# Optimization experiments

Hardware: AMD Instinct MI355X
Metric: run time of the kernel (lower is better)

Reference implementation:

```python
import jax, jax.numpy as jnp
import numpy as np

N_NODES = 50000
N_EDGES = 800000
DIMS = [128, 128, 128, 64]  # in, hid1, hid2, out
EPS = 1e-12


def setup_inputs() -> dict:
    key = jax.random.key(0)
    ks = jax.random.split(key, 32)
    inp = {
        "x": jax.random.normal(ks[0], (N_NODES, DIMS[0]), dtype=jnp.float32),
        "edge_src": jax.random.randint(ks[1], (N_EDGES,), 0, N_NODES),
        "edge_dst": jax.random.randint(ks[2], (N_EDGES,), 0, N_NODES),
    }
    k = 3
    for l in range(3):
        din, dout = DIMS[l], DIMS[l + 1]
        s_in = 1.0 / np.sqrt(din)
        inp[f"Wp{l+1}"] = jax.random.uniform(ks[k], (din, din), jnp.float32, -s_in, s_in); k += 1
        inp[f"bp{l+1}"] = jax.random.uniform(ks[k], (din,), jnp.float32, -s_in, s_in); k += 1
        inp[f"Ws{l+1}"] = jax.random.uniform(ks[k], (din, dout), jnp.float32, -s_in, s_in); k += 1
        inp[f"Wn{l+1}"] = jax.random.uniform(ks[k], (din, dout), jnp.float32, -s_in, s_in); k += 1
        inp[f"b{l+1}"] = jnp.zeros((dout,), jnp.float32); k += 1
    return inp


def _sage_pool_layer(x, src, dst, Wp, bp, Ws, Wn, b):
    # per-edge: relu(fc_pool(x_src)); [E, din]
    m = jax.nn.relu(x[src] @ Wp + bp)
    # max-pool over in-neighbors of each dst node; [N, din]
    pooled = jax.ops.segment_max(m, dst, num_segments=x.shape[0])
    deg = jax.ops.segment_sum(jnp.ones((dst.shape[0],), x.dtype), dst,
                              num_segments=x.shape[0])
    pooled = jnp.where(deg[:, None] > 0, pooled, 0.0)  # zero-degree -> 0 (DGL)
    return x @ Ws + pooled @ Wn + b


def _l2norm_relu(h):
    n = jnp.sqrt(jnp.sum(h * h, axis=1, keepdims=True))
    return jax.nn.relu(h / jnp.maximum(n, EPS))


def reference(x, edge_src, edge_dst,
              Wp1, bp1, Ws1, Wn1, b1,
              Wp2, bp2, Ws2, Wn2, b2,
              Wp3, bp3, Ws3, Wn3, b3):
    h = _l2norm_relu(_sage_pool_layer(x, edge_src, edge_dst, Wp1, bp1, Ws1, Wn1, b1))
    h = _l2norm_relu(_sage_pool_layer(h, edge_src, edge_dst, Wp2, bp2, Ws2, Wn2, b2))
    h = _l2norm_relu(_sage_pool_layer(h, edge_src, edge_dst, Wp3, bp3, Ws3, Wn3, b3))
    return h
```

## Files before the change

### kernel.cpp

```cpp
#include <hip/hip_runtime.h>
#include <math.h>

#define N_NODES 50000
#define N_EDGES 800000
#define CAP 64
#define RANGES 8
#define NODES_PER_RANGE 6250
#define CSRB 1024
#define GEMMB 782
#define LROW 136

typedef __attribute__((ext_vector_type(8))) short short8;
typedef __attribute__((ext_vector_type(2))) short short2v;
typedef __attribute__((ext_vector_type(4))) float f32x4;

__device__ __forceinline__ unsigned short f2bf(float f) {
    unsigned int u = __float_as_uint(f);
    return (unsigned short)((u + 0x7FFFu + ((u >> 16) & 1u)) >> 16);
}

template <bool F32>
__device__ __forceinline__ short8 loadA(const void* A, int off) {
    short8 r;
    if (F32) {
        const float* p = (const float*)A + off;
        float4 f0 = *(const float4*)p;
        float4 f1 = *(const float4*)(p + 4);
        r[0] = (short)f2bf(f0.x); r[1] = (short)f2bf(f0.y);
        r[2] = (short)f2bf(f0.z); r[3] = (short)f2bf(f0.w);
        r[4] = (short)f2bf(f1.x); r[5] = (short)f2bf(f1.y);
        r[6] = (short)f2bf(f1.z); r[7] = (short)f2bf(f1.w);
    } else {
        r = *(const short8*)((const unsigned short*)A + off);
    }
    return r;
}

struct WDescs { const float* W[9]; int N[9]; };

__global__ __launch_bounds__(256) void prep_kernel(
    WDescs wd, unsigned short* __restrict__ Wpk, int* __restrict__ deg)
{
    const int nthr = gridDim.x * 256;
    const int tid = blockIdx.x * 256 + threadIdx.x;
    for (int id = tid; id < 9 * 16384; id += nthr) {
        int mi = id >> 14;
        int loc = id & 16383;
        int N = wd.N[mi];
        if (loc < 128 * N) {
            int c = loc / (N * 32);
            int n = (loc - c * N * 32) >> 5;
            int k = c * 32 + (loc & 31);
            Wpk[mi * 16384 + loc] = f2bf(wd.W[mi][k * N + n]);
        }
    }
    for (int i = tid; i < N_NODES; i += nthr) deg[i] = 0;
}

__global__ __launch_bounds__(256) void mix_kernel(
    const int* __restrict__ esrc, const int* __restrict__ edst,
    int* __restrict__ deg, unsigned short* __restrict__ csr16,
    const float* __restrict__ x, const unsigned short* __restrict__ Wp1,
    const float* __restrict__ bp1, unsigned short* __restrict__ Y)
{
    if (blockIdx.x < CSRB) {
        int range = blockIdx.x & (RANGES - 1);
        for (int cb = blockIdx.x >> 3; cb < N_EDGES / 256; cb += CSRB / 8) {
            int e = cb * 256 + threadIdx.x;
            int d = edst[e];
            if ((unsigned)(d - range * NODES_PER_RANGE) < (unsigned)NODES_PER_RANGE) {
                int r = atomicAdd(&deg[d], 1);
                if (r < CAP) csr16[(d << 6) + r] = (unsigned short)esrc[e];
            }
        }
        return;
    }
    const int tile = blockIdx.x - CSRB;
    const int lane = threadIdx.x & 63;
    const int wv = threadIdx.x >> 6;
    const int cl = lane & 15;
    const int quad = lane >> 4;
    const int rowBase = tile * 64 + wv * 16;
    const int ar = min(rowBase + cl, N_NODES - 1);
    const int bLane = cl * 32 + quad * 8;

    f32x4 acc[8];
    #pragma unroll
    for (int t = 0; t < 8; ++t) acc[t] = (f32x4){0.f, 0.f, 0.f, 0.f};

    #pragma unroll
    for (int c = 0; c < 4; ++c) {
        short8 af = loadA<true>(x, ar * 128 + c * 32 + quad * 8);
        const unsigned short* Bc = Wp1 + c * 4096 + bLane;
        #pragma unroll
        for (int t = 0; t < 8; ++t) {
            short8 bf = *(const short8*)(Bc + t * 512);
            acc[t] = __builtin_amdgcn_mfma_f32_16x16x32_bf16(af, bf, acc[t], 0, 0, 0);
        }
    }
    const int row0 = rowBase + quad * 4;
    #pragma unroll
    for (int t = 0; t < 8; ++t) {
        float bc = bp1[t * 16 + cl];
        #pragma unroll
        for (int g = 0; g < 4; ++g) {
            int r = row0 + g;
            if (r < N_NODES)
                Y[r * 128 + t * 16 + cl] = f2bf(fmaxf(acc[t][g] + bc, 0.0f));
        }
    }
}

template <bool A0F32, bool LAST>
__global__ __launch_bounds__(256) void pd_kernel(
    const void* __restrict__ A0,
    const unsigned short* __restrict__ B0, const unsigned short* __restrict__ B1,
    const float* __restrict__ bias,
    const unsigned short* __restrict__ Yin, const int* __restrict__ deg,
    const unsigned short* __restrict__ csr16,
    unsigned short* __restrict__ outH, float* __restrict__ outF,
    const unsigned short* __restrict__ Bnext, const float* __restrict__ bnext,
    unsigned short* __restrict__ Yout)
{
    constexpr int NT = LAST ? 4 : 8;
    constexpr int N = NT * 16;
    __shared__ unsigned short lds[4][16 * LROW];

    const int lane = threadIdx.x & 63;
    const int wv = threadIdx.x >> 6;
    const int cl = lane & 15;
    const int quad = lane >> 4;
    const int tile = blockIdx.x;
    const int nodeBase = tile * 64 + wv * 16;
    unsigned short* plw = &lds[wv][0];

    {
        const unsigned short* yb = Yin + 2 * lane;
        for (int j = 0; j < 16; ++j) {
            int n = min(nodeBase + j, N_NODES - 1);
            int e0 = n << 6;
            int e1 = e0 + min(deg[n], CAP);
            short2v acc = (short2v){0, 0};
            int e = e0;
            for (; e + 8 <= e1; e += 8) {
                int s0 = csr16[e + 0], s1 = csr16[e + 1];
                int s2 = csr16[e + 2], s3 = csr16[e + 3];
                int s4 = csr16[e + 4], s5 = csr16[e + 5];
                int s6 = csr16[e + 6], s7 = csr16[e + 7];
                short2v v0 = *(const short2v*)(yb + (s0 << 7));
                short2v v1 = *(const short2v*)(yb + (s1 << 7));
                short2v v2 = *(const short2v*)(yb + (s2 << 7));
                short2v v3 = *(const short2v*)(yb + (s3 << 7));
                short2v v4 = *(const short2v*)(yb + (s4 << 7));
                short2v v5 = *(const short2v*)(yb + (s5 << 7));
                short2v v6 = *(const short2v*)(yb + (s6 << 7));
                short2v v7 = *(const short2v*)(yb + (s7 << 7));
                acc = __builtin_elementwise_max(acc, v0);
                acc = __builtin_elementwise_max(acc, v1);
                acc = __builtin_elementwise_max(acc, v2);
                acc = __builtin_elementwise_max(acc, v3);
                acc = __builtin_elementwise_max(acc, v4);
                acc = __builtin_elementwise_max(acc, v5);
                acc = __builtin_elementwise_max(acc, v6);
                acc = __builtin_elementwise_max(acc, v7);
            }
            for (; e < e1; ++e) {
                int s = csr16[e];
                short2v v = *(const short2v*)(yb + (s << 7));
                acc = __builtin_elementwise_max(acc, v);
            }
            *(short2v*)(plw + j * LROW + 2 * lane) = acc;
        }
    }

    const int ar = min(nodeBase + cl, N_NODES - 1);
    const int bLane = cl * 32 + quad * 8;
    f32x4 acc[NT];
    #pragma unroll
    for (int t = 0; t < NT; ++t) acc[t] = (f32x4){0.f, 0.f, 0.f, 0.f};

    #pragma unroll
    for (int c = 0; c < 4; ++c) {
        short8 a0 = loadA<A0F32>(A0, ar * 128 + c * 32 + quad * 8);
        short8 a1 = *(const short8*)(plw + cl * LROW + c * 32 + quad * 8);
        const unsigned short* B0c = B0 + c * (N * 32) + bLane;
        const unsigned short* B1c = B1 + c * (N * 32) + bLane;
        #pragma unroll
        for (int t = 0; t < NT; ++t) {
            short8 bf = *(const short8*)(B0c + t * 512);
            acc[t] = __builtin_amdgcn_mfma_f32_16x16x32_bf16(a0, bf, acc[t], 0, 0, 0);
        }
        #pragma unroll
        for (int t = 0; t < NT; ++t) {
            short8 bf = *(const short8*)(B1c + t * 512);
            acc[t] = __builtin_amdgcn_mfma_f32_16x16x32_bf16(a1, bf, acc[t], 0, 0, 0);
        }
    }

    #pragma unroll
    for (int t = 0; t < NT; ++t) {
        float bc = bias[t * 16 + cl];
        #pragma unroll
        for (int g = 0; g < 4; ++g) acc[t][g] += bc;
    }

    float inv[4];
    #pragma unroll
    for (int g = 0; g < 4; ++g) {
        float s = 0.f;
        #pragma unroll
        for (int t = 0; t < NT; ++t) s += acc[t][g] * acc[t][g];
        s += __shfl_xor(s, 1, 64);
        s += __shfl_xor(s, 2, 64);
        s += __shfl_xor(s, 4, 64);
        s += __shfl_xor(s, 8, 64);
        inv[g] = 1.0f / fmaxf(sqrtf(s), 1e-12f);
    }

    const int row0 = nodeBase + quad * 4;

    if (LAST) {
        #pragma unroll
        for (int t = 0; t < NT; ++t)
            #pragma unroll
            for (int g = 0; g < 4; ++g) {
                int r = row0 + g;
                if (r < N_NODES)
                    outF[r * N + t * 16 + cl] = fmaxf(acc[t][g] * inv[g], 0.0f);
            }
        return;
    }

    #pragma unroll
    for (int t = 0; t < NT; ++t)
        #pragma unroll
        for (int g = 0; g < 4; ++g) {
            int r = row0 + g;
            unsigned short h = f2bf(fmaxf(acc[t][g] * inv[g], 0.0f));
            if (r < N_NODES) outH[r * 128 + t * 16 + cl] = h;
            plw[(quad * 4 + g) * LROW + t * 16 + cl] = h;
        }

    f32x4 ya[8];
    #pragma unroll
    for (int t = 0; t < 8; ++t) ya[t] = (f32x4){0.f, 0.f, 0.f, 0.f};
    #pragma unroll
    for (int c = 0; c < 4; ++c) {
        short8 af = *(const short8*)(plw + cl * LROW + c * 32 + quad * 8);
        const unsigned short* Bc = Bnext + c * 4096 + bLane;
        #pragma unroll
        for (int t = 0; t < 8; ++t) {
            short8 bf = *(const short8*)(Bc + t * 512);
            ya[t] = __builtin_amdgcn_mfma_f32_16x16x32_bf16(af, bf, ya[t], 0, 0, 0);
        }
    }
    #pragma unroll
    for (int t = 0; t < 8; ++t) {
        float bc = bnext[t * 16 + cl];
        #pragma unroll
        for (int g = 0; g < 4; ++g) {
            int r = row0 + g;
            if (r < N_NODES)
                Yout[r * 128 + t * 16 + cl] = f2bf(fmaxf(ya[t][g] + bc, 0.0f));
        }
    }
}

extern "C" void kernel_launch(void* const* d_in, const int* in_sizes, int n_in,
                              void* d_out, int out_size, void* d_ws, size_t ws_size,
                              hipStream_t stream) {
    const float* x    = (const float*)d_in[0];
    const int*   esrc = (const int*)d_in[1];
    const int*   edst = (const int*)d_in[2];
    const float* Wp[3], *bp[3], *Ws[3], *Wn[3], *bb[3];
    for (int l = 0; l < 3; ++l) {
        Wp[l] = (const float*)d_in[3 + 5 * l];
        bp[l] = (const float*)d_in[4 + 5 * l];
        Ws[l] = (const float*)d_in[5 + 5 * l];
        Wn[l] = (const float*)d_in[6 + 5 * l];
        bb[l] = (const float*)d_in[7 + 5 * l];
    }

    const int NF = N_NODES * 128;
    unsigned short* YA  = (unsigned short*)d_ws;
    unsigned short* YB  = YA + NF;
    unsigned short* H1  = YB + NF;
    unsigned short* H2  = H1 + NF;
    unsigned short* Wpk = H2 + NF;
    int* deg = (int*)(Wpk + 9 * 16384);
    unsigned short* csr16 = (unsigned short*)(deg + N_NODES);

    auto WH = [&](int i) { return Wpk + i * 16384; };

    WDescs wd;
    wd.W[0] = Wp[0]; wd.N[0] = 128;
    wd.W[1] = Ws[0]; wd.N[1] = 128;
    wd.W[2] = Wn[0]; wd.N[2] = 128;
    wd.W[3] = Wp[1]; wd.N[3] = 128;
    wd.W[4] = Ws[1]; wd.N[4] = 128;
    wd.W[5] = Wn[1]; wd.N[5] = 128;
    wd.W[6] = Wp[2]; wd.N[6] = 128;
    wd.W[7] = Ws[2]; wd.N[7] = 64;
    wd.W[8] = Wn[2]; wd.N[8] = 64;

    prep_kernel<<<576, 256, 0, stream>>>(wd, Wpk, deg);
    mix_kernel<<<CSRB + GEMMB, 256, 0, stream>>>(esrc, edst, deg, csr16,
                                                 x, WH(0), bp[0], YA);
    pd_kernel<true, false><<<GEMMB, 256, 0, stream>>>(
        x, WH(1), WH(2), bb[0], YA, deg, csr16, H1, nullptr, WH(3), bp[1], YB);
    pd_kernel<false, false><<<GEMMB, 256, 0, stream>>>(
        H1, WH(4), WH(5), bb[1], YB, deg, csr16, H2, nullptr, WH(6), bp[2], YA);
    pd_kernel<false, true><<<GEMMB, 256, 0, stream>>>(
        H2, WH(7), WH(8), bb[2], YA, deg, csr16, nullptr, (float*)d_out,
        nullptr, nullptr, nullptr);
}
```

Measured before the change: 390.8 us.

## Split neighbor max-pool into separate per-node kernel before dual GEMM

The neighbor max-pooling gather is pulled out of the fused pool+GEMM kernel into its own kernel. That kernel gives each node a wavefront and launches 12500 blocks, so many more gathers are in flight than in the 782-block fused kernel, where each wave walked 16 nodes one after another. The GEMM kernel then reads the pooled rows from a global buffer instead of LDS. The cost is an extra global write and read of the pooled tensor per layer, plus three more kernel launches.

```diff
diff --git a/kernel.cpp b/kernel.cpp
--- a/kernel.cpp
+++ b/kernel.cpp
@@ -111,13 +111,55 @@
     }
 }
 
+__global__ __launch_bounds__(256) void pool_max8(
+    const unsigned short* __restrict__ y, const int* __restrict__ deg,
+    const unsigned short* __restrict__ csr16, unsigned short* __restrict__ pool)
+{
+    const int wv = threadIdx.x >> 6;
+    const int d = threadIdx.x & 63;
+    const int n = blockIdx.x * 4 + wv;
+    const int e0 = n << 6;
+    const int e1 = e0 + min(deg[n], CAP);
+    const unsigned short* yb = y + 2 * d;
+
+    short2v acc = (short2v){0, 0};
+    int e = e0;
+    for (; e + 8 <= e1; e += 8) {
+        int s0 = csr16[e + 0], s1 = csr16[e + 1];
+        int s2 = csr16[e + 2], s3 = csr16[e + 3];
+        int s4 = csr16[e + 4], s5 = csr16[e + 5];
+        int s6 = csr16[e + 6], s7 = csr16[e + 7];
+        short2v v0 = *(const short2v*)(yb + (s0 << 7));
+        short2v v1 = *(const short2v*)(yb + (s1 << 7));
+        short2v v2 = *(const short2v*)(yb + (s2 << 7));
+        short2v v3 = *(const short2v*)(yb + (s3 << 7));
+        short2v v4 = *(const short2v*)(yb + (s4 << 7));
+        short2v v5 = *(const short2v*)(yb + (s5 << 7));
+        short2v v6 = *(const short2v*)(yb + (s6 << 7));
+        short2v v7 = *(const short2v*)(yb + (s7 << 7));
+        acc = __builtin_elementwise_max(acc, v0);
+        acc = __builtin_elementwise_max(acc, v1);
+        acc = __builtin_elementwise_max(acc, v2);
+        acc = __builtin_elementwise_max(acc, v3);
+        acc = __builtin_elementwise_max(acc, v4);
+        acc = __builtin_elementwise_max(acc, v5);
+        acc = __builtin_elementwise_max(acc, v6);
+        acc = __builtin_elementwise_max(acc, v7);
+    }
+    for (; e < e1; ++e) {
+        int s = csr16[e];
+        short2v v = *(const short2v*)(yb + (s << 7));
+        acc = __builtin_elementwise_max(acc, v);
+    }
+    *(short2v*)(pool + n * 128 + 2 * d) = acc;
+}
+
 template <bool A0F32, bool LAST>
-__global__ __launch_bounds__(256) void pd_kernel(
+__global__ __launch_bounds__(256) void dualy_kernel(
     const void* __restrict__ A0,
     const unsigned short* __restrict__ B0, const unsigned short* __restrict__ B1,
     const float* __restrict__ bias,
-    const unsigned short* __restrict__ Yin, const int* __restrict__ deg,
-    const unsigned short* __restrict__ csr16,
+    const unsigned short* __restrict__ PL,
     unsigned short* __restrict__ outH, float* __restrict__ outF,
     const unsigned short* __restrict__ Bnext, const float* __restrict__ bnext,
     unsigned short* __restrict__ Yout)
@@ -130,59 +172,21 @@
     const int wv = threadIdx.x >> 6;
     const int cl = lane & 15;
     const int quad = lane >> 4;
-    const int tile = blockIdx.x;
-    const int nodeBase = tile * 64 + wv * 16;
+    const int nodeBase = blockIdx.x * 64 + wv * 16;
     unsigned short* plw = &lds[wv][0];
 
-    {
-        const unsigned short* yb = Yin + 2 * lane;
-        for (int j = 0; j < 16; ++j) {
-            int n = min(nodeBase + j, N_NODES - 1);
-            int e0 = n << 6;
-            int e1 = e0 + min(deg[n], CAP);
-            short2v acc = (short2v){0, 0};
-            int e = e0;
-            for (; e + 8 <= e1; e += 8) {
-                int s0 = csr16[e + 0], s1 = csr16[e + 1];
-                int s2 = csr16[e + 2], s3 = csr16[e + 3];
-                int s4 = csr16[e + 4], s5 = csr16[e + 5];
-                int s6 = csr16[e + 6], s7 = csr16[e + 7];
-                short2v v0 = *(const short2v*)(yb + (s0 << 7));
-                short2v v1 = *(const short2v*)(yb + (s1 << 7));
-                short2v v2 = *(const short2v*)(yb + (s2 << 7));
-                short2v v3 = *(const short2v*)(yb + (s3 << 7));
-                short2v v4 = *(const short2v*)(yb + (s4 << 7));
-                short2v v5 = *(const short2v*)(yb + (s5 << 7));
-                short2v v6 = *(const short2v*)(yb + (s6 << 7));
-                short2v v7 = *(const short2v*)(yb + (s7 << 7));
-                acc = __builtin_elementwise_max(acc, v0);
-                acc = __builtin_elementwise_max(acc, v1);
-                acc = __builtin_elementwise_max(acc, v2);
-                acc = __builtin_elementwise_max(acc, v3);
-                acc = __builtin_elementwise_max(acc, v4);
-                acc = __builtin_elementwise_max(acc, v5);
-                acc = __builtin_elementwise_max(acc, v6);
-                acc = __builtin_elementwise_max(acc, v7);
-            }
-            for (; e < e1; ++e) {
-                int s = csr16[e];
-                short2v v = *(const short2v*)(yb + (s << 7));
-                acc = __builtin_elementwise_max(acc, v);
-            }
-            *(short2v*)(plw + j * LROW + 2 * lane) = acc;
-        }
-    }
-
     const int ar = min(nodeBase + cl, N_NODES - 1);
+    const int aBase = ar * 128 + quad * 8;
     const int bLane = cl * 32 + quad * 8;
+
     f32x4 acc[NT];
     #pragma unroll
     for (int t = 0; t < NT; ++t) acc[t] = (f32x4){0.f, 0.f, 0.f, 0.f};
 
     #pragma unroll
     for (int c = 0; c < 4; ++c) {
-        short8 a0 = loadA<A0F32>(A0, ar * 128 + c * 32 + quad * 8);
-        short8 a1 = *(const short8*)(plw + cl * LROW + c * 32 + quad * 8);
+        short8 a0 = loadA<A0F32>(A0, aBase + c * 32);
+        short8 a1 = *(const short8*)(PL + aBase + c * 32);
         const unsigned short* B0c = B0 + c * (N * 32) + bLane;
         const unsigned short* B1c = B1 + c * (N * 32) + bLane;
         #pragma unroll
@@ -284,7 +288,8 @@
     const int NF = N_NODES * 128;
     unsigned short* YA  = (unsigned short*)d_ws;
     unsigned short* YB  = YA + NF;
-    unsigned short* H1  = YB + NF;
+    unsigned short* PL  = YB + NF;
+    unsigned short* H1  = PL + NF;
     unsigned short* H2  = H1 + NF;
     unsigned short* Wpk = H2 + NF;
     int* deg = (int*)(Wpk + 9 * 16384);
@@ -303,14 +308,19 @@
     wd.W[7] = Ws[2]; wd.N[7] = 64;
     wd.W[8] = Wn[2]; wd.N[8] = 64;
 
+    const int poolBlocks = N_NODES / 4;
+
     prep_kernel<<<576, 256, 0, stream>>>(wd, Wpk, deg);
     mix_kernel<<<CSRB + GEMMB, 256, 0, stream>>>(esrc, edst, deg, csr16,
                                                  x, WH(0), bp[0], YA);
-    pd_kernel<true, false><<<GEMMB, 256, 0, stream>>>(
-        x, WH(1), WH(2), bb[0], YA, deg, csr16, H1, nullptr, WH(3), bp[1], YB);
-    pd_kernel<false, false><<<GEMMB, 256, 0, stream>>>(
-        H1, WH(4), WH(5), bb[1], YB, deg, csr16, H2, nullptr, WH(6), bp[2], YA);
-    pd_kernel<false, true><<<GEMMB, 256, 0, stream>>>(
-        H2, WH(7), WH(8), bb[2], YA, deg, csr16, nullptr, (float*)d_out,
+    pool_max8<<<poolBlocks, 256, 0, stream>>>(YA, deg, csr16, PL);
+    dualy_kernel<true, false><<<GEMMB, 256, 0, stream>>>(
+        x, WH(1), WH(2), bb[0], PL, H1, nullptr, WH(3), bp[1], YB);
+    pool_max8<<<poolBlocks, 256, 0, stream>>>(YB, deg, csr16, PL);
+    dualy_kernel<false, false><<<GEMMB, 256, 0, stream>>>(
+        H1, WH(4), WH(5), bb[1], PL, H2, nullptr, WH(6), bp[2], YA);
+    pool_max8<<<poolBlocks, 256, 0, stream>>>(YA, deg, csr16, PL);
+    dualy_kernel<false, true><<<GEMMB, 256, 0, stream>>>(
+        H2, WH(7), WH(8), bb[2], PL, nullptr, (float*)d_out,
         nullptr, nullptr, nullptr);
 }
```

Measured after the change: 349.8 us. 1.12x faster.
